# Kernel tuning notes

Measured on AMD Instinct MI355X. Metric: run time of the kernel, lower is better.

## Reference

```python
import jax, jax.numpy as jnp
import numpy as np

TAU = 0.5

def setup_inputs() -> dict:
    key = jax.random.key(0)
    kx, ky = jax.random.split(key)
    B, H = 8192, 256
    x = jax.random.normal(kx, (B, H), dtype=jnp.float32)
    y = jax.random.normal(ky, (B, H), dtype=jnp.float32)
    return {"x": x, "y": y}

def reference(x, y):
    # L2-normalize rows
    x_norm = x / jnp.linalg.norm(x, axis=1, keepdims=True)
    y_norm = y / jnp.linalg.norm(y, axis=1, keepdims=True)
    xy_norm = jnp.concatenate([x_norm, y_norm], axis=0)  # [2N, H]
    yx_norm = jnp.concatenate([y_norm, x_norm], axis=0)  # [2N, H]
    # [2N, 2N] cosine-similarity matrix (dominant memory traffic)
    sim_mat_1 = xy_norm @ xy_norm.T
    exp_mat = jnp.exp(sim_mat_1 / TAU)
    exp_row_sum = jnp.sum(exp_mat, axis=1)
    exp_diag = jnp.diagonal(exp_mat)
    denominator = exp_row_sum - exp_diag
    # diag(xy_norm @ yx_norm.T) is the row-wise dot product (avoids redundant NxN matmul)
    pos_sim = jnp.sum(xy_norm * yx_norm, axis=1)
    numerator = jnp.exp(pos_sim / TAU)
    nt_xent = -jnp.log(numerator / denominator)
    return jnp.mean(nt_xent)
```

## Files before the change

### kernel.cpp

```cpp
#include <hip/hip_runtime.h>
#include <hip/hip_bf16.h>
#include <math.h>

constexpr int NROWS = 8192;
constexpr int HDIM  = 256;
constexpr int N2    = 16384;
constexpr int TM    = 256;
constexpr int BKB   = 64;
constexpr int NCHUNK = HDIM / BKB;
constexpr int PIECEB = TM * BKB;
constexpr int NTILE = N2 / TM;
constexpr int NBLK  = NTILE * (NTILE + 1) / 2;

constexpr float PRESCALE = 1.69864357f;

typedef __attribute__((ext_vector_type(4))) float floatx4;

__device__ __forceinline__ void async_copy16(const void* gptr, void* lptr) {
    __builtin_amdgcn_global_load_lds(
        (const __attribute__((address_space(1))) unsigned int*)gptr,
        (__attribute__((address_space(3))) unsigned int*)lptr, 16, 0, 0);
}

#define WAIT_VM2()   __builtin_amdgcn_s_waitcnt(0x0F72)
#define WAIT_VM0()   __builtin_amdgcn_s_waitcnt(0x0F70)
#define MEMFENCE()   __asm__ __volatile__("" ::: "memory")
#define RAW_BARRIER() do { MEMFENCE(); __builtin_amdgcn_s_barrier(); MEMFENCE(); } while (0)

#define DPP_ROW_SHL_ADD(v, CTRL) do {                                        \
    union { float f; int i; } _u, _r; _u.f = (v);                            \
    _r.i = __builtin_amdgcn_update_dpp(0, _u.i, (CTRL), 0xF, 0xF, true);     \
    (v) += _r.f; } while (0)

__device__ __forceinline__ unsigned int f32_to_e4m3(float f) {
    const float a = fabsf(f);
    const unsigned int s = f < 0.f ? 0x80u : 0u;
    if (a < 0.015625f) {
        int mm = (int)rintf(a * 512.0f);
        if (mm == 8) return s | 0x08u;
        return s | (unsigned int)mm;
    }
    int e; const float fr = frexpf(a, &e);
    int mm = (int)rintf(fr * 16.0f) - 8;
    int E  = e + 6;
    if (mm == 8) { mm = 0; E += 1; }
    if (E > 15) { E = 15; mm = 6; }
    return s | (unsigned int)((E << 3) | mm);
}

__global__ __launch_bounds__(256) void normalize_kernel(
    const float* __restrict__ x, const float* __restrict__ y,
    unsigned char* __restrict__ Zb, float* __restrict__ pos,
    float* __restrict__ rowsum, float* __restrict__ out)
{
    const int wave = threadIdx.x >> 6, lane = threadIdx.x & 63;
    const int row  = blockIdx.x * 4 + wave;

    const float4 xv = ((const float4*)x)[row * 64 + lane];
    const float4 yv = ((const float4*)y)[row * 64 + lane];

    float sx  = xv.x*xv.x + xv.y*xv.y + xv.z*xv.z + xv.w*xv.w;
    float sy  = yv.x*yv.x + yv.y*yv.y + yv.z*yv.z + yv.w*yv.w;
    float sxy = xv.x*yv.x + xv.y*yv.y + xv.z*yv.z + xv.w*yv.w;
    #pragma unroll
    for (int m = 1; m < 64; m <<= 1) {
        sx  += __shfl_xor(sx,  m);
        sy  += __shfl_xor(sy,  m);
        sxy += __shfl_xor(sxy, m);
    }
    const float rxn = rsqrtf(sx), ryn = rsqrtf(sy);
    const float rx = rxn * PRESCALE, ry = ryn * PRESCALE;

    const unsigned int px =
        f32_to_e4m3(xv.x * rx)        | (f32_to_e4m3(xv.y * rx) << 8) |
        (f32_to_e4m3(xv.z * rx) << 16) | (f32_to_e4m3(xv.w * rx) << 24);
    const unsigned int py =
        f32_to_e4m3(yv.x * ry)        | (f32_to_e4m3(yv.y * ry) << 8) |
        (f32_to_e4m3(yv.z * ry) << 16) | (f32_to_e4m3(yv.w * ry) << 24);

    ((unsigned int*)Zb)[row * 64 + lane]             = px;
    ((unsigned int*)Zb)[(row + NROWS) * 64 + lane]   = py;

    if (lane == 0) {
        const float p = sxy * rxn * ryn;
        pos[row]         = p;
        pos[row + NROWS] = p;
    }
    const int gt = blockIdx.x * 256 + threadIdx.x;
    if (gt < N2) rowsum[gt] = 0.f;
    if (gt == 0) out[0] = 0.f;
}

__global__ __launch_bounds__(1024, 4) void simgemm_kernel(
    const unsigned char* __restrict__ Zb, float* __restrict__ rowsum)
{
    const int b = blockIdx.x;
    const int k = b & 7;
    const int m = b >> 3;
    int bi, bj;
    if (m < 36) {
        int ti = (int)((17.0f - sqrtf(289.0f - 8.0f * (float)m)) * 0.5f);
        if (m < ti * (17 - ti) / 2) ti--;
        else if (m >= (ti + 1) * (16 - ti) / 2) ti++;
        const int tj = ti + (m - ti * (17 - ti) / 2);
        bi = k * 8 + ti;
        bj = k * 8 + tj;
    } else {
        const int m2 = m - 36;
        const int hh = m2 >> 5;
        const int r  = m2 & 31;
        const int h  = hh * 8 + k;
        const int q  = h >> 1;
        const int sub = h & 1;
        int gi = 0;
        #pragma unroll
        for (int t = 6; t > 0; --t)
            if (q >= t * (15 - t) / 2) { gi = t; break; }
        const int gj = gi + 1 + (q - gi * (15 - gi) / 2);
        bi = gi * 8 + sub * 4 + (r >> 3);
        bj = gj * 8 + (r & 7);
    }
    const bool diag = (bi == bj);

    __shared__ alignas(16) char tiles[6 * PIECEB];
    __shared__ float rs[TM];
    __shared__ float cs[TM];

    const int tid  = threadIdx.x;
    const int wave = tid >> 6;
    const int lane = tid & 63;
    const int wm   = wave & 3;
    const int wn   = wave >> 2;
    const int g    = lane >> 4;
    const int m15  = lane & 15;

    if (tid < TM) { rs[tid] = 0.f; cs[tid] = 0.f; }

    const int st_r0 = wave * 16 + (lane >> 2);
    const int st_c  = (lane & 3) ^ ((lane >> 3) & 3);
    const unsigned char* gA0 = Zb + (size_t)(bi * TM + st_r0) * HDIM + st_c * 16;
    const unsigned char* gB0 = Zb + (size_t)(bj * TM + st_r0) * HDIM + st_c * 16;

    const int xr = (m15 >> 1) & 3;
    const int s0 = g >> 1;
    const int ha = (g & 1) * 8;
    const int off0 = ((s0 ^ xr) * 16) + ha;
    const int off1 = (((2 + s0) ^ xr) * 16) + ha;
    const int rowA = (wm * 64 + m15) * BKB;
    const int rowB = (wn * 64 + m15) * BKB;

    floatx4 acc[4][4] = {};

    #define STAGE(ck)  do {                                                  \
        const int _o = ((ck) % 3) * 2 * PIECEB;                              \
        async_copy16(gA0 + (ck) * BKB, tiles + _o + (wave * 16) * BKB);      \
        async_copy16(gB0 + (ck) * BKB,                                       \
                     tiles + _o + PIECEB + (wave * 16) * BKB);               \
    } while (0)

    STAGE(0);

    #pragma unroll
    for (int s = 0; s < NCHUNK; ++s) {
        if (s + 1 < NCHUNK) { STAGE(s + 1); WAIT_VM2(); }
        else                { WAIT_VM0(); }
        RAW_BARRIER();

        const char* bA = tiles + (s % 3) * 2 * PIECEB;
        const char* bB = bA + PIECEB;
        long af[2][4], bfr[2][4];
        #pragma unroll
        for (int ks = 0; ks < 2; ++ks) {
            const int off = ks ? off1 : off0;
            #pragma unroll
            for (int f = 0; f < 4; ++f) {
                af[ks][f]  = *(const long*)(bA + rowA + f * 16 * BKB + off);
                bfr[ks][f] = *(const long*)(bB + rowB + f * 16 * BKB + off);
            }
        }
        __builtin_amdgcn_s_setprio(1);
        #pragma unroll
        for (int ks = 0; ks < 2; ++ks)
            #pragma unroll
            for (int fm = 0; fm < 4; ++fm)
                #pragma unroll
                for (int fn = 0; fn < 4; ++fn)
                    acc[fm][fn] = __builtin_amdgcn_mfma_f32_16x16x32_fp8_fp8(
                        af[ks][fm], bfr[ks][fn], acc[fm][fn], 0, 0, 0);
        __builtin_amdgcn_s_setprio(0);
    }
    #undef STAGE

    float rp[4][4] = {{0.f}};
    float cp[4]    = {0.f};

    if (!diag) {
        #pragma unroll
        for (int fm = 0; fm < 4; ++fm)
            #pragma unroll
            for (int fn = 0; fn < 4; ++fn) {
                const floatx4 a = acc[fm][fn];
                #pragma unroll
                for (int q = 0; q < 4; ++q) {
                    const float e = __builtin_amdgcn_exp2f(a[q]);
                    rp[fm][q] += e;
                    cp[fn]    += e;
                }
            }
    } else {
        #pragma unroll
        for (int fm = 0; fm < 4; ++fm)
            #pragma unroll
            for (int fn = 0; fn < 4; ++fn) {
                const floatx4 a = acc[fm][fn];
                const int cl = wn * 64 + fn * 16 + m15;
                #pragma unroll
                for (int q = 0; q < 4; ++q) {
                    const int rl = wm * 64 + fm * 16 + g * 4 + q;
                    float e = __builtin_amdgcn_exp2f(a[q]);
                    if (cl <= rl) e = 0.f;
                    rp[fm][q] += e;
                    cp[fn]    += e;
                }
            }
    }

    #pragma unroll
    for (int fm = 0; fm < 4; ++fm)
        #pragma unroll
        for (int q = 0; q < 4; ++q) {
            float v = rp[fm][q];
            DPP_ROW_SHL_ADD(v, 0x101);
            DPP_ROW_SHL_ADD(v, 0x102);
            DPP_ROW_SHL_ADD(v, 0x104);
            DPP_ROW_SHL_ADD(v, 0x108);
            rp[fm][q] = v;
        }
    if (m15 == 0) {
        #pragma unroll
        for (int fm = 0; fm < 4; ++fm)
            #pragma unroll
            for (int q = 0; q < 4; ++q)
                atomicAdd(&rs[wm * 64 + fm * 16 + g * 4 + q], rp[fm][q]);
    }

    #pragma unroll
    for (int mask = 16; mask < 64; mask <<= 1)
        #pragma unroll
        for (int fn = 0; fn < 4; ++fn)
            cp[fn] += __shfl_xor(cp[fn], mask);
    if (g == 0) {
        #pragma unroll
        for (int fn = 0; fn < 4; ++fn)
            atomicAdd(&cs[wn * 64 + fn * 16 + m15], cp[fn]);
    }

    __syncthreads();
    if (tid < TM) {
        atomicAdd(&rowsum[(size_t)bi * TM + tid], rs[tid]);
        atomicAdd(&rowsum[(size_t)bj * TM + tid], cs[tid]);
    }
}

__global__ __launch_bounds__(1024) void finalize_kernel(
    const float* __restrict__ rowsum, const float* __restrict__ pos,
    float* __restrict__ out)
{
    const int i = threadIdx.x + blockIdx.x * 1024;
    float s = logf(rowsum[i]) - 2.0f * pos[i];
    #pragma unroll
    for (int off = 32; off; off >>= 1) s += __shfl_down(s, off);
    __shared__ float sh[16];
    const int lt = threadIdx.x;
    if ((lt & 63) == 0) sh[lt >> 6] = s;
    __syncthreads();
    if (lt == 0) {
        float tot = 0.f;
        #pragma unroll
        for (int w = 0; w < 16; ++w) tot += sh[w];
        atomicAdd(out, tot / (float)N2);
    }
}

extern "C" void kernel_launch(void* const* d_in, const int* in_sizes, int n_in,
                              void* d_out, int out_size, void* d_ws, size_t ws_size,
                              hipStream_t stream)
{
    const float* x = (const float*)d_in[0];
    const float* y = (const float*)d_in[1];

    unsigned char* Zb = (unsigned char*)d_ws;
    float* rowsum = (float*)((char*)d_ws + (size_t)N2 * HDIM);
    float* pos    = rowsum + N2;

    normalize_kernel<<<NROWS / 4, 256, 0, stream>>>(x, y, Zb, pos, rowsum, (float*)d_out);
    simgemm_kernel<<<NBLK, 1024, 0, stream>>>(Zb, rowsum);
    finalize_kernel<<<N2 / 1024, 1024, 0, stream>>>(rowsum, pos, (float*)d_out);
}
```

Measured before the change: 153.3 us.

## Load full K tiles into LDS at once instead of triple-buffered chunk pipeline

Replaces the three-stage pipelined loading of 64-byte K chunks with a single bulk async load of both full 256x256 fp8 tiles (128 KB LDS), one wait and one barrier, then an 8-step MFMA loop over K. This removes the per-chunk barriers and waitcnts. In exchange there is no overlap between global loads and MFMA work within a block, LDS use grows, and occupancy is likely limited to one block per CU. The row layout and XOR swizzle change to match full-width rows.

```diff
diff --git a/kernel.cpp b/kernel.cpp
--- a/kernel.cpp
+++ b/kernel.cpp
@@ -6,9 +6,7 @@
 constexpr int HDIM  = 256;
 constexpr int N2    = 16384;
 constexpr int TM    = 256;
-constexpr int BKB   = 64;
-constexpr int NCHUNK = HDIM / BKB;
-constexpr int PIECEB = TM * BKB;
+constexpr int TILEB = TM * HDIM;
 constexpr int NTILE = N2 / TM;
 constexpr int NBLK  = NTILE * (NTILE + 1) / 2;
 
@@ -22,7 +20,6 @@
         (__attribute__((address_space(3))) unsigned int*)lptr, 16, 0, 0);
 }
 
-#define WAIT_VM2()   __builtin_amdgcn_s_waitcnt(0x0F72)
 #define WAIT_VM0()   __builtin_amdgcn_s_waitcnt(0x0F70)
 #define MEMFENCE()   __asm__ __volatile__("" ::: "memory")
 #define RAW_BARRIER() do { MEMFENCE(); __builtin_amdgcn_s_barrier(); MEMFENCE(); } while (0)
@@ -122,7 +119,7 @@
     }
     const bool diag = (bi == bj);
 
-    __shared__ alignas(16) char tiles[6 * PIECEB];
+    __shared__ alignas(16) unsigned char tiles[2 * TILEB];
     __shared__ float rs[TM];
     __shared__ float cs[TM];
 
@@ -136,60 +133,54 @@
 
     if (tid < TM) { rs[tid] = 0.f; cs[tid] = 0.f; }
 
-    const int st_r0 = wave * 16 + (lane >> 2);
-    const int st_c  = (lane & 3) ^ ((lane >> 3) & 3);
-    const unsigned char* gA0 = Zb + (size_t)(bi * TM + st_r0) * HDIM + st_c * 16;
-    const unsigned char* gB0 = Zb + (size_t)(bj * TM + st_r0) * HDIM + st_c * 16;
-
-    const int xr = (m15 >> 1) & 3;
-    const int s0 = g >> 1;
-    const int ha = (g & 1) * 8;
-    const int off0 = ((s0 ^ xr) * 16) + ha;
-    const int off1 = (((2 + s0) ^ xr) * 16) + ha;
-    const int rowA = (wm * 64 + m15) * BKB;
-    const int rowB = (wn * 64 + m15) * BKB;
+    const int xr_e = (lane >> 5) & 3;
+    const int xr_o = (2 + (lane >> 5)) & 3;
+    const int win  = ((lane & 15) >> 2) * 64;
+    const int soff_e = win + (((lane & 3) ^ xr_e) * 16);
+    const int soff_o = win + (((lane & 3) ^ xr_o) * 16);
+    const unsigned char* gA = Zb + (size_t)(bi * TM + wave * 16 + (lane >> 4)) * HDIM;
+    const unsigned char* gB = Zb + (size_t)(bj * TM + wave * 16 + (lane >> 4)) * HDIM;
+    unsigned char* lA = tiles + (wave * 16) * HDIM;
+    unsigned char* lB = tiles + TILEB + (wave * 16) * HDIM;
+
+    async_copy16(gA + 0 * 1024 + soff_e, lA + 0 * 1024);
+    async_copy16(gA + 1 * 1024 + soff_o, lA + 1 * 1024);
+    async_copy16(gA + 2 * 1024 + soff_e, lA + 2 * 1024);
+    async_copy16(gA + 3 * 1024 + soff_o, lA + 3 * 1024);
+    async_copy16(gB + 0 * 1024 + soff_e, lB + 0 * 1024);
+    async_copy16(gB + 1 * 1024 + soff_o, lB + 1 * 1024);
+    async_copy16(gB + 2 * 1024 + soff_e, lB + 2 * 1024);
+    async_copy16(gB + 3 * 1024 + soff_o, lB + 3 * 1024);
+
+    WAIT_VM0();
+    RAW_BARRIER();
+
+    const int xr  = (m15 >> 1) & 3;
+    const int slg = g >> 1;
+    const int ha  = (g & 1) * 8;
+    const int rowA = (wm * 64 + m15) * HDIM;
+    const int rowB = (wn * 64 + m15) * HDIM;
+    const unsigned char* bA = tiles;
+    const unsigned char* bB = tiles + TILEB;
 
     floatx4 acc[4][4] = {};
 
-    #define STAGE(ck)  do {                                                  \
-        const int _o = ((ck) % 3) * 2 * PIECEB;                              \
-        async_copy16(gA0 + (ck) * BKB, tiles + _o + (wave * 16) * BKB);      \
-        async_copy16(gB0 + (ck) * BKB,                                       \
-                     tiles + _o + PIECEB + (wave * 16) * BKB);               \
-    } while (0)
-
-    STAGE(0);
-
-    #pragma unroll
-    for (int s = 0; s < NCHUNK; ++s) {
-        if (s + 1 < NCHUNK) { STAGE(s + 1); WAIT_VM2(); }
-        else                { WAIT_VM0(); }
-        RAW_BARRIER();
-
-        const char* bA = tiles + (s % 3) * 2 * PIECEB;
-        const char* bB = bA + PIECEB;
-        long af[2][4], bfr[2][4];
-        #pragma unroll
-        for (int ks = 0; ks < 2; ++ks) {
-            const int off = ks ? off1 : off0;
-            #pragma unroll
-            for (int f = 0; f < 4; ++f) {
-                af[ks][f]  = *(const long*)(bA + rowA + f * 16 * BKB + off);
-                bfr[ks][f] = *(const long*)(bB + rowB + f * 16 * BKB + off);
-            }
+    #pragma unroll
+    for (int t = 0; t < 8; ++t) {
+        const int off = (t >> 1) * 64 + (((((t & 1) << 1) + slg) ^ xr) * 16) + ha;
+        long af[4], bfr[4];
+        #pragma unroll
+        for (int f = 0; f < 4; ++f) {
+            af[f]  = *(const long*)(bA + rowA + f * 16 * HDIM + off);
+            bfr[f] = *(const long*)(bB + rowB + f * 16 * HDIM + off);
         }
-        __builtin_amdgcn_s_setprio(1);
-        #pragma unroll
-        for (int ks = 0; ks < 2; ++ks)
-            #pragma unroll
-            for (int fm = 0; fm < 4; ++fm)
-                #pragma unroll
-                for (int fn = 0; fn < 4; ++fn)
-                    acc[fm][fn] = __builtin_amdgcn_mfma_f32_16x16x32_fp8_fp8(
-                        af[ks][fm], bfr[ks][fn], acc[fm][fn], 0, 0, 0);
-        __builtin_amdgcn_s_setprio(0);
-    }
-    #undef STAGE
+        #pragma unroll
+        for (int fm = 0; fm < 4; ++fm)
+            #pragma unroll
+            for (int fn = 0; fn < 4; ++fn)
+                acc[fm][fn] = __builtin_amdgcn_mfma_f32_16x16x32_fp8_fp8(
+                    af[fm], bfr[fn], acc[fm][fn], 0, 0, 0);
+    }
 
     float rp[4][4] = {{0.f}};
     float cp[4]    = {0.f};
```

New measurement: 180.3 us. +17.6%, slower.
